# Optimization experiments

Measured on AMD Instinct MI355X. Metric: run time of the kernel, lower is better.

## Reference

```python
import jax, jax.numpy as jnp
import numpy as np

WAY = 5
SHOT = 5
NEIGHBOR_K = 3


def setup_inputs() -> dict:
    key = jax.random.key(0)
    k1, k2 = jax.random.split(key)
    x1 = jax.random.normal(k1, (75, 640, 21, 21), dtype=jnp.float32)   # queries
    x2 = jax.random.normal(k2, (25, 640, 21, 21), dtype=jnp.float32)   # support (way*shot)
    return {"x1": x1, "x2": x2}


def reference(x1, x2):
    Q, C, H, W = x1.shape
    S = x2.shape[0]  # way * shot
    HW = H * W

    # queries: [Q, C, HW] -> [Q, HW, C], L2-normalize each local descriptor
    q = jnp.transpose(x1.reshape(Q, C, HW), (0, 2, 1))
    q = q / jnp.linalg.norm(q, axis=2, keepdims=True)

    # support: [S, HW, C], normalize, regroup per class: [way, shot*HW, C]
    s = jnp.transpose(x2.reshape(S, C, HW), (0, 2, 1))
    s = s / jnp.linalg.norm(s, axis=2, keepdims=True)
    s = s.reshape(WAY, SHOT * HW, C)

    # cosine similarity of every query descriptor vs every class descriptor
    # [Q, way, HW, shot*HW]
    sim = jnp.einsum('qmc,wnc->qwmn', q, s)

    # top-k neighbors per query descriptor along class-descriptor axis, then sum
    topk_vals, _ = jax.lax.top_k(sim, NEIGHBOR_K)   # [Q, way, HW, k]
    img2class_sim = jnp.sum(topk_vals, axis=(2, 3))  # [Q, way]
    return img2class_sim
```

## Files before the change

### kernel.cpp

```cpp
#include <hip/hip_runtime.h>

typedef unsigned char u8;
typedef int i32x4 __attribute__((ext_vector_type(4)));
typedef int i32x16 __attribute__((ext_vector_type(16)));

#define C_DIM 640
#define HW_DIM 441
#define QN 75
#define SN 25
#define WAYS 5
#define MROWS 33075
#define MCH   64
#define MBLK  517
#define MPAD  33088
#define NWAY  2205
#define NPAD  2304
#define BN    256
#define NT    9
#define INV_Q2 (1.0f / 16129.0f)
#define NEGINF (-2147483647 - 1)

__device__ __forceinline__ void glds16(const void* g, void* l) {
  __builtin_amdgcn_global_load_lds(
      (__attribute__((address_space(1))) unsigned int*)g,
      (__attribute__((address_space(3))) unsigned int*)l, 16, 0, 0);
}

__global__ void zero_pad(u8* __restrict__ A8, u8* __restrict__ S8,
                         float* __restrict__ out) {
  int i = blockIdx.x * 256 + threadIdx.x;
  if (i < 8320) {
    A8[(size_t)MROWS * C_DIM + i] = 0;
    return;
  }
  i -= 8320;
  if (i < 316800) {
    const int w = i / 63360;
    const int r = i % 63360;
    S8[((size_t)w * NPAD + NWAY) * C_DIM + r] = 0;
    return;
  }
  i -= 316800;
  if (i < QN * WAYS) out[i] = 0.f;
}

__global__ __launch_bounds__(256)
void prep_norm_transpose(const float* __restrict__ src, u8* __restrict__ dst,
                         int support) {
  const int bid = blockIdx.x;
  const int img = bid / 7;
  const int mt = bid % 7;
  const int m0 = mt * 64;
  const int t = threadIdx.x;
  const int mloc = t & 63;
  const int cpart = t >> 6;
  const int m = m0 + mloc;
  const int m_eff = (m < HW_DIM) ? m : (HW_DIM - 1);
  const float* base = src + (size_t)img * (C_DIM * HW_DIM);

  float ss = 0.f;
  const int c0 = cpart * 160;
  for (int c = c0; c < c0 + 160; ++c) {
    float v = base[(size_t)c * HW_DIM + m_eff];
    ss += v * v;
  }
  __shared__ float red[256];
  __shared__ float inv[64];
  red[t] = ss;
  __syncthreads();
  if (t < 64) {
    float s4 = red[t] + red[t + 64] + red[t + 128] + red[t + 192];
    inv[t] = rsqrtf(s4) * 127.0f;
  }
  __syncthreads();

  size_t drow0;
  if (support) {
    const int w = img / 5, shot = img % 5;
    drow0 = (size_t)w * NPAD + (size_t)shot * HW_DIM;
  } else {
    drow0 = (size_t)img * HW_DIM;
  }

  __shared__ __align__(16) u8 T[64][80];
  const float iv = inv[mloc];
  const int mw = t >> 2;
  const int cg = t & 3;
  const int m_out = m0 + mw;

  for (int ct = 0; ct < 10; ++ct) {
    int q[16];
#pragma unroll
    for (int ci = 0; ci < 16; ++ci) {
      const int c = ct * 64 + cpart * 16 + ci;
      q[ci] = __float2int_rn(base[(size_t)c * HW_DIM + m_eff] * iv);
    }
    __syncthreads();
    uint4 w;
    w.x = (q[0] & 255) | ((q[1] & 255) << 8) | ((q[2] & 255) << 16) | ((q[3] & 255) << 24);
    w.y = (q[4] & 255) | ((q[5] & 255) << 8) | ((q[6] & 255) << 16) | ((q[7] & 255) << 24);
    w.z = (q[8] & 255) | ((q[9] & 255) << 8) | ((q[10] & 255) << 16) | ((q[11] & 255) << 24);
    w.w = (q[12] & 255) | ((q[13] & 255) << 8) | ((q[14] & 255) << 16) | ((q[15] & 255) << 24);
    *(uint4*)&T[mloc][cpart * 16] = w;
    __syncthreads();
    if (m_out < HW_DIM) {
      const uint4 v = *(const uint4*)&T[mw][cg * 16];
      *(uint4*)(dst + (drow0 + m_out) * C_DIM + ct * 64 + cg * 16) = v;
    }
  }
}

__global__ __launch_bounds__(256, 2)
void simtopk(const u8* __restrict__ A8, const u8* __restrict__ S8,
             float* __restrict__ out) {
  __shared__ __align__(16) u8 Bs[2][BN * 128];
  __shared__ float qsum[2];

  const int bid = blockIdx.x;
  const int way = bid / MBLK;
  const int mc = bid % MBLK;
  const int R0 = mc * MCH;
  const int tid = threadIdx.x;
  const int lane = tid & 63;
  const int wv = tid >> 6;
  const int wm = (wv >> 1) * 32;
  const int nh = wv & 1;
  const int wnB = nh * 128;
  const int r5 = lane & 31;
  const int h = lane >> 5;

  if (tid < 2) qsum[tid] = 0.f;

  const u8* Sway = S8 + (size_t)way * NPAD * C_DIM;

  i32x4 a[20];
  {
    const u8* Arow = A8 + (size_t)(R0 + wm + r5) * C_DIM + h * 16;
#pragma unroll
    for (int ks = 0; ks < 20; ++ks)
      a[ks] = *(const i32x4*)(Arow + ks * 32);
  }

  const unsigned brow =
      (unsigned)((lane >> 3) * 640 + (((lane & 7) ^ (lane >> 3)) * 16));
#pragma unroll
  for (int j = 0; j < 8; ++j) {
    const int st = wv * 8 + j;
    glds16(Sway + (unsigned)st * (8 * 640) + brow, Bs[0] + st * 1024);
  }

  int bBase[4], pqs[4];
#pragma unroll
  for (int ni = 0; ni < 4; ++ni)
    bBase[ni] = (wnB + ni * 32 + r5) * 128;
#pragma unroll
  for (int s = 0; s < 4; ++s)
    pqs[s] = ((2 * s + h) ^ (r5 & 7)) * 16;

  i32x16 acc[4];
#pragma unroll
  for (int ni = 0; ni < 4; ++ni)
#pragma unroll
    for (int g = 0; g < 16; ++g) acc[ni][g] = 0;

  int t0[16], t1[16], t2[16];
#pragma unroll
  for (int r = 0; r < 16; ++r) { t0[r] = NEGINF; t1[r] = NEGINF; t2[r] = NEGINF; }

  int p = 0;
  for (int nt = 0; nt < NT; ++nt) {
#pragma unroll
    for (int kt = 0; kt < 5; ++kt) {
      __syncthreads();

      if (!(nt == NT - 1 && kt == 4)) {
        const int nt1 = (kt == 4) ? nt + 1 : nt;
        const int kt1 = (kt == 4) ? 0 : kt + 1;
        const unsigned off =
            (unsigned)nt1 * (BN * C_DIM) + (unsigned)(kt1 * 128);
#pragma unroll
        for (int j = 0; j < 8; ++j) {
          const int st = wv * 8 + j;
          glds16(Sway + (unsigned)st * (8 * 640) + brow + off,
                 Bs[p ^ 1] + st * 1024);
        }
      }

      const u8* Bp = Bs[p];
#pragma unroll
      for (int s = 0; s < 4; ++s) {
        const i32x4 av = a[kt * 4 + s];
        i32x4 b0 = *(const i32x4*)(Bp + bBase[0] + pqs[s]);
        i32x4 b1 = *(const i32x4*)(Bp + bBase[1] + pqs[s]);
        i32x4 b2 = *(const i32x4*)(Bp + bBase[2] + pqs[s]);
        i32x4 b3 = *(const i32x4*)(Bp + bBase[3] + pqs[s]);
        acc[0] = __builtin_amdgcn_mfma_i32_32x32x32_i8(av, b0, acc[0], 0, 0, 0);
        acc[1] = __builtin_amdgcn_mfma_i32_32x32x32_i8(av, b1, acc[1], 0, 0, 0);
        acc[2] = __builtin_amdgcn_mfma_i32_32x32x32_i8(av, b2, acc[2], 0, 0, 0);
        acc[3] = __builtin_amdgcn_mfma_i32_32x32x32_i8(av, b3, acc[3], 0, 0, 0);
      }
      p ^= 1;
    }

    const bool lastT = (nt == NT - 1);
#pragma unroll
    for (int ni = 0; ni < 4; ++ni) {
      const int ncol = nt * BN + wnB + ni * 32 + r5;
      const bool bad = lastT && (ncol >= NWAY);
#pragma unroll
      for (int g = 0; g < 16; ++g) {
        int v = acc[ni][g];
        if (bad) v = NEGINF;
        t2[g] = max(t2[g], min(v, t1[g]));
        t1[g] = max(t1[g], min(v, t0[g]));
        t0[g] = max(t0[g], v);
        acc[ni][g] = 0;
      }
    }
  }

#pragma unroll
  for (int d = 1; d <= 2; d <<= 1) {
#pragma unroll
    for (int r = 0; r < 16; ++r) {
      const int o0 = __shfl_xor(t0[r], d);
      const int o1 = __shfl_xor(t1[r], d);
      const int o2 = __shfl_xor(t2[r], d);
      t2[r] = max(t2[r], min(o0, t1[r]));
      t1[r] = max(t1[r], min(o0, t0[r]));
      t0[r] = max(t0[r], o0);
      t2[r] = max(t2[r], min(o1, t1[r]));
      t1[r] = max(t1[r], min(o1, t0[r]));
      t0[r] = max(t0[r], o1);
      t2[r] = max(t2[r], min(o2, t1[r]));
      t1[r] = max(t1[r], min(o2, t0[r]));
      t0[r] = max(t0[r], o2);
    }
  }

  __syncthreads();
  int* part = (int*)&Bs[0][0];
  if ((r5 & 3) == 0) {
    const int grp = nh * 8 + (r5 >> 2);
#pragma unroll
    for (int r = 0; r < 16; ++r) {
      const int row_local = wm + (r & 3) + 8 * (r >> 2) + 4 * h;
      i32x4 v;
      v[0] = t0[r]; v[1] = t1[r]; v[2] = t2[r]; v[3] = NEGINF;
      *(i32x4*)&part[(grp * MCH + row_local) * 4] = v;
    }
  }
  __syncthreads();
  if (tid < MCH) {
    const int grow = R0 + tid;
    if (grow < MROWS) {
      int a0 = NEGINF, a1 = NEGINF, a2 = NEGINF;
#pragma unroll 4
      for (int g = 0; g < 16; ++g) {
        const i32x4 v = *(const i32x4*)&part[(g * MCH + tid) * 4];
        a2 = max(a2, min(v[0], a1)); a1 = max(a1, min(v[0], a0)); a0 = max(a0, v[0]);
        a2 = max(a2, min(v[1], a1)); a1 = max(a1, min(v[1], a0)); a0 = max(a0, v[1]);
        a2 = max(a2, min(v[2], a1)); a1 = max(a1, min(v[2], a0)); a0 = max(a0, v[2]);
      }
      const float rs = (float)(a0 + a1 + a2) * INV_Q2;
      const int qq = grow / HW_DIM;
      atomicAdd(&qsum[qq - (R0 / HW_DIM)], rs);
    }
  }
  __syncthreads();
  if (tid < 2) {
    const int qq = R0 / HW_DIM + tid;
    if (qq < QN) atomicAdd(out + qq * WAYS + way, qsum[tid]);
  }
}

extern "C" void kernel_launch(void* const* d_in, const int* in_sizes, int n_in,
                              void* d_out, int out_size, void* d_ws, size_t ws_size,
                              hipStream_t stream) {
  const float* x1 = (const float*)d_in[0];
  const float* x2 = (const float*)d_in[1];
  float* out = (float*)d_out;
  u8* A8 = (u8*)d_ws;
  u8* S8 = (u8*)d_ws + (size_t)MPAD * C_DIM;

  hipLaunchKernelGGL(zero_pad, dim3(1272), dim3(256), 0, stream, A8, S8, out);
  hipLaunchKernelGGL(prep_norm_transpose, dim3(QN * 7), dim3(256), 0, stream,
                     x1, A8, 0);
  hipLaunchKernelGGL(prep_norm_transpose, dim3(SN * 7), dim3(256), 0, stream,
                     x2, S8, 1);
  hipLaunchKernelGGL(simtopk, dim3(WAYS * MBLK), dim3(256), 0, stream,
                     A8, S8, out);
}
```

Before: 539.9 us.

## Double M-tile per block to reuse B fragments and use med3 for top-3

Each block now covers 128 query rows instead of 64, and each wave holds two A row-fragments so every B fragment read from LDS feeds two MFMAs. This halves LDS reads and global support traffic per output and halves the number of blocks. The running top-3 update now uses v_med3_i32, the padding-column mask is applied only on the last tile, and the partial-result LDS buffer is XOR-swizzled to avoid bank conflicts. The cost is much higher register pressure, with launch bounds relaxed to one block per CU, and fewer blocks for the GPU to schedule.

```diff
diff --git a/kernel.cpp b/kernel.cpp
--- a/kernel.cpp
+++ b/kernel.cpp
@@ -10,9 +10,9 @@
 #define SN 25
 #define WAYS 5
 #define MROWS 33075
-#define MCH   64
-#define MBLK  517
-#define MPAD  33088
+#define MCH   128
+#define MBLK  259
+#define MPAD  33152
 #define NWAY  2205
 #define NPAD  2304
 #define BN    256
@@ -26,14 +26,20 @@
       (__attribute__((address_space(3))) unsigned int*)l, 16, 0, 0);
 }
 
+__device__ __forceinline__ int med3i(int a, int b, int c) {
+  int d;
+  asm("v_med3_i32 %0, %1, %2, %3" : "=v"(d) : "v"(a), "v"(b), "v"(c));
+  return d;
+}
+
 __global__ void zero_pad(u8* __restrict__ A8, u8* __restrict__ S8,
                          float* __restrict__ out) {
   int i = blockIdx.x * 256 + threadIdx.x;
-  if (i < 8320) {
+  if (i < 49280) {
     A8[(size_t)MROWS * C_DIM + i] = 0;
     return;
   }
-  i -= 8320;
+  i -= 49280;
   if (i < 316800) {
     const int w = i / 63360;
     const int r = i % 63360;
@@ -110,7 +116,7 @@
   }
 }
 
-__global__ __launch_bounds__(256, 2)
+__global__ __launch_bounds__(256, 1)
 void simtopk(const u8* __restrict__ A8, const u8* __restrict__ S8,
              float* __restrict__ out) {
   __shared__ __align__(16) u8 Bs[2][BN * 128];
@@ -123,7 +129,7 @@
   const int tid = threadIdx.x;
   const int lane = tid & 63;
   const int wv = tid >> 6;
-  const int wm = (wv >> 1) * 32;
+  const int wm = (wv >> 1) * 64;
   const int nh = wv & 1;
   const int wnB = nh * 128;
   const int r5 = lane & 31;
@@ -133,12 +139,14 @@
 
   const u8* Sway = S8 + (size_t)way * NPAD * C_DIM;
 
-  i32x4 a[20];
+  i32x4 a0[20], a1[20];
   {
-    const u8* Arow = A8 + (size_t)(R0 + wm + r5) * C_DIM + h * 16;
-#pragma unroll
-    for (int ks = 0; ks < 20; ++ks)
-      a[ks] = *(const i32x4*)(Arow + ks * 32);
+    const u8* Ar = A8 + (size_t)(R0 + wm + r5) * C_DIM + h * 16;
+#pragma unroll
+    for (int ks = 0; ks < 20; ++ks) {
+      a0[ks] = *(const i32x4*)(Ar + ks * 32);
+      a1[ks] = *(const i32x4*)(Ar + 32 * C_DIM + ks * 32);
+    }
   }
 
   const unsigned brow =
@@ -157,15 +165,17 @@
   for (int s = 0; s < 4; ++s)
     pqs[s] = ((2 * s + h) ^ (r5 & 7)) * 16;
 
-  i32x16 acc[4];
-#pragma unroll
-  for (int ni = 0; ni < 4; ++ni)
-#pragma unroll
-    for (int g = 0; g < 16; ++g) acc[ni][g] = 0;
-
-  int t0[16], t1[16], t2[16];
-#pragma unroll
-  for (int r = 0; r < 16; ++r) { t0[r] = NEGINF; t1[r] = NEGINF; t2[r] = NEGINF; }
+  i32x16 acc[2][4];
+#pragma unroll
+  for (int mi = 0; mi < 2; ++mi)
+#pragma unroll
+    for (int ni = 0; ni < 4; ++ni)
+#pragma unroll
+      for (int g = 0; g < 16; ++g) acc[mi][ni][g] = 0;
+
+  int t0[32], t1[32], t2[32];
+#pragma unroll
+  for (int r = 0; r < 32; ++r) { t0[r] = NEGINF; t1[r] = NEGINF; t2[r] = NEGINF; }
 
   int p = 0;
   for (int nt = 0; nt < NT; ++nt) {
@@ -189,51 +199,73 @@
       const u8* Bp = Bs[p];
 #pragma unroll
       for (int s = 0; s < 4; ++s) {
-        const i32x4 av = a[kt * 4 + s];
-        i32x4 b0 = *(const i32x4*)(Bp + bBase[0] + pqs[s]);
-        i32x4 b1 = *(const i32x4*)(Bp + bBase[1] + pqs[s]);
-        i32x4 b2 = *(const i32x4*)(Bp + bBase[2] + pqs[s]);
-        i32x4 b3 = *(const i32x4*)(Bp + bBase[3] + pqs[s]);
-        acc[0] = __builtin_amdgcn_mfma_i32_32x32x32_i8(av, b0, acc[0], 0, 0, 0);
-        acc[1] = __builtin_amdgcn_mfma_i32_32x32x32_i8(av, b1, acc[1], 0, 0, 0);
-        acc[2] = __builtin_amdgcn_mfma_i32_32x32x32_i8(av, b2, acc[2], 0, 0, 0);
-        acc[3] = __builtin_amdgcn_mfma_i32_32x32x32_i8(av, b3, acc[3], 0, 0, 0);
+        const i32x4 av0 = a0[kt * 4 + s];
+        const i32x4 av1 = a1[kt * 4 + s];
+        const i32x4 b0v = *(const i32x4*)(Bp + bBase[0] + pqs[s]);
+        const i32x4 b1v = *(const i32x4*)(Bp + bBase[1] + pqs[s]);
+        const i32x4 b2v = *(const i32x4*)(Bp + bBase[2] + pqs[s]);
+        const i32x4 b3v = *(const i32x4*)(Bp + bBase[3] + pqs[s]);
+        acc[0][0] = __builtin_amdgcn_mfma_i32_32x32x32_i8(av0, b0v, acc[0][0], 0, 0, 0);
+        acc[1][0] = __builtin_amdgcn_mfma_i32_32x32x32_i8(av1, b0v, acc[1][0], 0, 0, 0);
+        acc[0][1] = __builtin_amdgcn_mfma_i32_32x32x32_i8(av0, b1v, acc[0][1], 0, 0, 0);
+        acc[1][1] = __builtin_amdgcn_mfma_i32_32x32x32_i8(av1, b1v, acc[1][1], 0, 0, 0);
+        acc[0][2] = __builtin_amdgcn_mfma_i32_32x32x32_i8(av0, b2v, acc[0][2], 0, 0, 0);
+        acc[1][2] = __builtin_amdgcn_mfma_i32_32x32x32_i8(av1, b2v, acc[1][2], 0, 0, 0);
+        acc[0][3] = __builtin_amdgcn_mfma_i32_32x32x32_i8(av0, b3v, acc[0][3], 0, 0, 0);
+        acc[1][3] = __builtin_amdgcn_mfma_i32_32x32x32_i8(av1, b3v, acc[1][3], 0, 0, 0);
       }
       p ^= 1;
     }
 
-    const bool lastT = (nt == NT - 1);
-#pragma unroll
-    for (int ni = 0; ni < 4; ++ni) {
-      const int ncol = nt * BN + wnB + ni * 32 + r5;
-      const bool bad = lastT && (ncol >= NWAY);
-#pragma unroll
-      for (int g = 0; g < 16; ++g) {
-        int v = acc[ni][g];
-        if (bad) v = NEGINF;
-        t2[g] = max(t2[g], min(v, t1[g]));
-        t1[g] = max(t1[g], min(v, t0[g]));
-        t0[g] = max(t0[g], v);
-        acc[ni][g] = 0;
-      }
+    if (nt != NT - 1) {
+#pragma unroll
+      for (int mi = 0; mi < 2; ++mi)
+#pragma unroll
+        for (int ni = 0; ni < 4; ++ni)
+#pragma unroll
+          for (int g = 0; g < 16; ++g) {
+            const int v = acc[mi][ni][g];
+            const int r = mi * 16 + g;
+            t2[r] = med3i(v, t1[r], t2[r]);
+            t1[r] = med3i(v, t0[r], t1[r]);
+            t0[r] = max(t0[r], v);
+            acc[mi][ni][g] = 0;
+          }
+    } else {
+#pragma unroll
+      for (int mi = 0; mi < 2; ++mi)
+#pragma unroll
+        for (int ni = 0; ni < 4; ++ni) {
+          const int ncol = nt * BN + wnB + ni * 32 + r5;
+          const bool bad = (ncol >= NWAY);
+#pragma unroll
+          for (int g = 0; g < 16; ++g) {
+            int v = acc[mi][ni][g];
+            if (bad) v = NEGINF;
+            const int r = mi * 16 + g;
+            t2[r] = med3i(v, t1[r], t2[r]);
+            t1[r] = med3i(v, t0[r], t1[r]);
+            t0[r] = max(t0[r], v);
+          }
+        }
     }
   }
 
 #pragma unroll
   for (int d = 1; d <= 2; d <<= 1) {
 #pragma unroll
-    for (int r = 0; r < 16; ++r) {
+    for (int r = 0; r < 32; ++r) {
       const int o0 = __shfl_xor(t0[r], d);
       const int o1 = __shfl_xor(t1[r], d);
       const int o2 = __shfl_xor(t2[r], d);
-      t2[r] = max(t2[r], min(o0, t1[r]));
-      t1[r] = max(t1[r], min(o0, t0[r]));
+      t2[r] = med3i(o0, t1[r], t2[r]);
+      t1[r] = med3i(o0, t0[r], t1[r]);
       t0[r] = max(t0[r], o0);
-      t2[r] = max(t2[r], min(o1, t1[r]));
-      t1[r] = max(t1[r], min(o1, t0[r]));
+      t2[r] = med3i(o1, t1[r], t2[r]);
+      t1[r] = med3i(o1, t0[r], t1[r]);
       t0[r] = max(t0[r], o1);
-      t2[r] = max(t2[r], min(o2, t1[r]));
-      t1[r] = max(t1[r], min(o2, t0[r]));
+      t2[r] = med3i(o2, t1[r], t2[r]);
+      t1[r] = med3i(o2, t0[r], t1[r]);
       t0[r] = max(t0[r], o2);
     }
   }
@@ -243,26 +275,28 @@
   if ((r5 & 3) == 0) {
     const int grp = nh * 8 + (r5 >> 2);
 #pragma unroll
-    for (int r = 0; r < 16; ++r) {
-      const int row_local = wm + (r & 3) + 8 * (r >> 2) + 4 * h;
+    for (int r = 0; r < 32; ++r) {
+      const int mi = r >> 4;
+      const int g = r & 15;
+      const int row_local = wm + mi * 32 + (g & 3) + 8 * (g >> 2) + 4 * h;
       i32x4 v;
       v[0] = t0[r]; v[1] = t1[r]; v[2] = t2[r]; v[3] = NEGINF;
-      *(i32x4*)&part[(grp * MCH + row_local) * 4] = v;
+      *(i32x4*)&part[(grp * MCH + (row_local ^ (grp & 7))) * 4] = v;
     }
   }
   __syncthreads();
   if (tid < MCH) {
     const int grow = R0 + tid;
     if (grow < MROWS) {
-      int a0 = NEGINF, a1 = NEGINF, a2 = NEGINF;
+      int a0_ = NEGINF, a1_ = NEGINF, a2_ = NEGINF;
 #pragma unroll 4
       for (int g = 0; g < 16; ++g) {
-        const i32x4 v = *(const i32x4*)&part[(g * MCH + tid) * 4];
-        a2 = max(a2, min(v[0], a1)); a1 = max(a1, min(v[0], a0)); a0 = max(a0, v[0]);
-        a2 = max(a2, min(v[1], a1)); a1 = max(a1, min(v[1], a0)); a0 = max(a0, v[1]);
-        a2 = max(a2, min(v[2], a1)); a1 = max(a1, min(v[2], a0)); a0 = max(a0, v[2]);
+        const i32x4 v = *(const i32x4*)&part[(g * MCH + (tid ^ (g & 7))) * 4];
+        a2_ = med3i(v[0], a1_, a2_); a1_ = med3i(v[0], a0_, a1_); a0_ = max(a0_, v[0]);
+        a2_ = med3i(v[1], a1_, a2_); a1_ = med3i(v[1], a0_, a1_); a0_ = max(a0_, v[1]);
+        a2_ = med3i(v[2], a1_, a2_); a1_ = med3i(v[2], a0_, a1_); a0_ = max(a0_, v[2]);
       }
-      const float rs = (float)(a0 + a1 + a2) * INV_Q2;
+      const float rs = (float)(a0_ + a1_ + a2_) * INV_Q2;
       const int qq = grow / HW_DIM;
       atomicAdd(&qsum[qq - (R0 / HW_DIM)], rs);
     }
@@ -283,7 +317,7 @@
   u8* A8 = (u8*)d_ws;
   u8* S8 = (u8*)d_ws + (size_t)MPAD * C_DIM;
 
-  hipLaunchKernelGGL(zero_pad, dim3(1272), dim3(256), 0, stream, A8, S8, out);
+  hipLaunchKernelGGL(zero_pad, dim3(1432), dim3(256), 0, stream, A8, S8, out);
   hipLaunchKernelGGL(prep_norm_transpose, dim3(QN * 7), dim3(256), 0, stream,
                      x1, A8, 0);
   hipLaunchKernelGGL(prep_norm_transpose, dim3(SN * 7), dim3(256), 0, stream,
```

New measurement: 1.002 ms. 1.86x slower.
